# Optimization experiments

Measured on AMD Instinct MI355X. Metric: run time of the kernel, lower is better.

## Reference

```python
import itertools
import jax, jax.numpy as jnp
import numpy as np

# ---- config (mirrors init_kwargs) ----
BS = 8; H = 120; W = 160
RES = 5; ZRES = 5
MAP_SIZE_CM = 2400 // 2          # global_downscaling = 2 -> 1200 cm
VR = 100                          # vision_range
FOV = 79.0
NSEM = 16
CAT_THR = 5.0; EXP_THR = 1.0; MAP_THR = 1.0
AGENT_H = 0.88 * 100.0            # camera height in cm
MAX_H = int(360 / ZRES)           # 72
MIN_H = int(-40 / ZRES)           # -8
MAP_DIM = MAP_SIZE_CM // RES      # 240
XC = (W - 1.0) / 2.0
ZC = (H - 1.0) / 2.0
FL = (W / 2.0) / np.tan(np.deg2rad(FOV / 2.0))
D2R = 1.0 / 57.29577951308232


def splat_feat_nd(init_grid, feat, coords):
    """Trilinear splat-scatter. init_grid: (B,F,*gd); feat: (B,F,P); coords: (B,ndim,P) in [-1,1]."""
    B, Fc = init_grid.shape[:2]
    gd = init_grid.shape[2:]
    n = len(gd)
    grid_flat = init_grid.reshape(B, Fc, -1)
    pos_d, wts_d = [], []
    for d in range(n):
        pos = coords[:, d:d + 1, :] * (gd[d] / 2.0) + gd[d] / 2.0  # (B,1,P)
        pd, wd = [], []
        for ix in (0, 1):
            pos_ix = jnp.floor(pos) + ix
            safe = ((pos_ix > 0) & (pos_ix < gd[d])).astype(pos.dtype)
            wd.append((1.0 - jnp.abs(pos - pos_ix)) * safe)
            pd.append((pos_ix * safe).astype(jnp.int32))
        pos_d.append(pd); wts_d.append(wd)
    bidx = jnp.arange(B)[:, None, None]
    fidx = jnp.arange(Fc)[None, :, None]
    for comb in itertools.product((0, 1), repeat=n):
        idx = jnp.zeros_like(pos_d[0][0])
        w = jnp.ones_like(wts_d[0][0])
        for d in range(n):
            idx = idx * gd[d] + pos_d[d][comb[d]]
            w = w * wts_d[d][comb[d]]
        grid_flat = grid_flat.at[bidx, fidx, idx].add(feat * w)
    return jnp.round(grid_flat).reshape(init_grid.shape)


def affine_grid(theta, Ho, Wo):
    """torch F.affine_grid with align_corners=True. theta: (B,2,3) -> (B,Ho,Wo,2)."""
    xs = jnp.linspace(-1.0, 1.0, Wo)
    ys = jnp.linspace(-1.0, 1.0, Ho)
    Xg, Yg = jnp.meshgrid(xs, ys)
    base = jnp.stack([Xg, Yg, jnp.ones_like(Xg)], -1)  # (Ho,Wo,3)
    return jnp.einsum('hwk,bjk->bhwj', base, theta)


def grid_sample(img, grid):
    """Bilinear grid_sample, align_corners=True, zero padding. img: (B,C,Hi,Wi); grid: (B,Ho,Wo,2)."""
    B, C, Hi, Wi = img.shape
    x = (grid[..., 0] + 1.0) * (Wi - 1) / 2.0
    y = (grid[..., 1] + 1.0) * (Hi - 1) / 2.0
    x0 = jnp.floor(x); y0 = jnp.floor(y)
    bidx = jnp.arange(B)[:, None, None, None]
    cidx = jnp.arange(C)[None, :, None, None]

    def tap(ix, iy, w):
        valid = ((ix >= 0) & (ix < Wi) & (iy >= 0) & (iy < Hi)).astype(img.dtype)
        ixc = jnp.clip(ix, 0, Wi - 1).astype(jnp.int32)
        iyc = jnp.clip(iy, 0, Hi - 1).astype(jnp.int32)
        v = img[bidx, cidx, iyc[:, None], ixc[:, None]]  # (B,C,Ho,Wo)
        return v * (w * valid)[:, None]

    out = tap(x0, y0, (x0 + 1 - x) * (y0 + 1 - y))
    out = out + tap(x0 + 1, y0, (x - x0) * (y0 + 1 - y))
    out = out + tap(x0, y0 + 1, (x0 + 1 - x) * (y - y0))
    out = out + tap(x0 + 1, y0 + 1, (x - x0) * (y - y0))
    return out


def _forward(obs, pose_obs, maps_last, poses_last):
    B, c = obs.shape[0], obs.shape[1]
    depth = obs[:, 3]  # (B,H,W), cm

    # point cloud from depth (du.get_point_cloud_from_z_t, du_scale=1)
    gx = jnp.broadcast_to(jnp.arange(W, dtype=depth.dtype)[None, :], (H, W))
    gz = jnp.broadcast_to(jnp.arange(H - 1, -1, -1, dtype=depth.dtype)[:, None], (H, W))
    X = (gx - XC) * depth / FL
    Z = (gz - ZC) * depth / FL
    pc = jnp.stack([X, depth, Z], axis=-1)  # (B,H,W,3)

    # camera elevation rotation about x-axis (view_angles default to 0)
    elev = jnp.zeros((B,), depth.dtype)
    ce, se = jnp.cos(elev), jnp.sin(elev)
    z0 = jnp.zeros_like(ce); o1 = jnp.ones_like(ce)
    Rx = jnp.stack([o1, z0, z0, z0, ce, -se, z0, se, ce], -1).reshape(B, 3, 3)
    pc = jnp.einsum('bhwk,bjk->bhwj', pc, Rx)
    pc = pc.at[..., 2].add(AGENT_H)

    # shift pose: rotate about z by (pi/2 - pi/2) = 0, translate x by vr*res//2
    ang = np.pi / 2.0 - np.pi / 2.0
    Rz = jnp.array([[np.cos(ang), -np.sin(ang), 0.0],
                    [np.sin(ang), np.cos(ang), 0.0],
                    [0.0, 0.0, 1.0]], depth.dtype)
    pc = jnp.einsum('bhwk,jk->bhwj', pc, Rz)
    pc = pc.at[..., 0].add(VR * RES // 2)

    # normalize to [-1,1] voxel coords
    xs = (pc[..., 0] / RES - VR // 2.0) / VR * 2.0
    ys = (pc[..., 1] / RES - VR // 2.0) / VR * 2.0
    zs = (pc[..., 2] / ZRES - (MAX_H + MIN_H) // 2.0) / (MAX_H - MIN_H) * 2.0
    coords = jnp.stack([xs, ys, zs], 1).reshape(B, 3, H * W)

    # feat: channel 0 = ones (occupancy), rest = semantic masks (AvgPool2d(1) = identity)
    feat = jnp.concatenate([jnp.ones((B, 1, H * W), obs.dtype),
                            obs[:, 4:].reshape(B, NSEM, H * W)], axis=1)

    init_grid = jnp.zeros((B, 1 + NSEM, VR, VR, MAX_H - MIN_H), obs.dtype)
    voxels = splat_feat_nd(init_grid, feat, coords).swapaxes(2, 3)

    min_z = int(5 / ZRES - MIN_H)                  # 9
    max_z = int((AGENT_H + 1 + 50) / ZRES - MIN_H)  # 35
    agent_height_proj = voxels[..., min_z:max_z].sum(4)
    all_height_proj = voxels.sum(4)

    fp_map_pred = jnp.clip(agent_height_proj[:, 0:1] / MAP_THR, 0.0, 1.0)
    fp_exp_pred = jnp.clip(all_height_proj[:, 0:1] / EXP_THR, 0.0, 1.0)

    agent_view = jnp.zeros((B, c, MAP_DIM, MAP_DIM), obs.dtype)
    x1 = MAP_SIZE_CM // (RES * 2) - VR // 2; x2 = x1 + VR
    y1 = MAP_SIZE_CM // (RES * 2); y2 = y1 + VR
    agent_view = agent_view.at[:, 0:1, y1:y2, x1:x2].set(fp_map_pred)
    agent_view = agent_view.at[:, 1:2, y1:y2, x1:x2].set(fp_exp_pred)
    agent_view = agent_view.at[:, 4:, y1:y2, x1:x2].set(
        jnp.clip(agent_height_proj[:, 1:] / CAT_THR, 0.0, 1.0))
    # cat_pred_threshold > 5.0 branch is False (threshold == 5.0)

    # pose update (note: torch mutates poses_last in place -> pose_pred aliases current_poses)
    th = poses_last[:, 2] * D2R
    ny = poses_last[:, 1] + pose_obs[:, 0] * jnp.sin(th) + pose_obs[:, 1] * jnp.cos(th)
    nx = poses_last[:, 0] + pose_obs[:, 0] * jnp.cos(th) - pose_obs[:, 1] * jnp.sin(th)
    nt = poses_last[:, 2] + pose_obs[:, 2] * 57.29577951308232
    nt = jnp.fmod(nt - 180.0, 360.0) + 180.0
    nt = jnp.fmod(nt + 180.0, 360.0) - 180.0
    current_poses = jnp.stack([nx, ny, nt], 1)

    st = jax.lax.stop_gradient(current_poses)  # .clone().detach()
    half = MAP_SIZE_CM // (RES * 2)
    st_xy = -(st[:, :2] * 100.0 / RES - half) / half
    st_t = 90.0 - st[:, 2]
    cos_t = jnp.cos(st_t * np.pi / 180.0); sin_t = jnp.sin(st_t * np.pi / 180.0)
    z0 = jnp.zeros_like(cos_t); o1 = jnp.ones_like(cos_t)
    theta1 = jnp.stack([jnp.stack([cos_t, -sin_t, z0], 1),
                        jnp.stack([sin_t, cos_t, z0], 1)], 1)
    theta2 = jnp.stack([jnp.stack([o1, z0, st_xy[:, 0]], 1),
                        jnp.stack([z0, o1, st_xy[:, 1]], 1)], 1)
    rot_grid = affine_grid(theta1, MAP_DIM, MAP_DIM)
    trans_grid = affine_grid(theta2, MAP_DIM, MAP_DIM)
    rotated = grid_sample(agent_view, rot_grid)
    translated = grid_sample(rotated, trans_grid)

    map_pred = jnp.maximum(maps_last, translated)
    return (fp_map_pred, map_pred, current_poses, current_poses)


def setup_inputs() -> dict:
    key = jax.random.key(0)
    k1, k2, k3, k4, k5, k6 = jax.random.split(key, 6)
    obs = jax.random.uniform(k1, (BS, 4 + NSEM, H, W), jnp.float32)
    depth = 50.0 + 300.0 * jax.random.uniform(k2, (BS, H, W), jnp.float32)  # cm
    obs = obs.at[:, 3].set(depth)
    pose_obs = 0.1 * jax.random.normal(k3, (BS, 3), jnp.float32)
    maps_last = jax.random.uniform(k4, (BS, 4 + NSEM, MAP_DIM, MAP_DIM), jnp.float32)
    xy = 4.0 + 4.0 * jax.random.uniform(k5, (BS, 2), jnp.float32)  # meters, inside 12m map
    th = 360.0 * jax.random.uniform(k6, (BS, 1), jnp.float32) - 180.0
    poses_last = jnp.concatenate([xy, th], 1)
    return {"obs": obs, "pose_obs": pose_obs, "maps_last": maps_last, "poses_last": poses_last}


def reference(obs, pose_obs, maps_last, poses_last):
    return _forward(obs, pose_obs, maps_last, poses_last)
```

## Files before the change

kernel.cpp:

```cpp
#include <hip/hip_runtime.h>
#include <math.h>

#define NB 8
#define NH 120
#define NW 160
#define HW (NH*NW)
#define NSEM 16
#define NCH 20
#define VR 100
#define NZ 80
#define NZP 40
#define ZLO 9
#define ZHI 35
#define NZS (ZHI-ZLO)
#define MD 240
#define PC 20
#define YW 64
#define YOFF 8
#define QS0    256.0f
#define QS0INV 0.00390625f
#define QS2    8.0f
#define QS2INV 0.125f
#define PXB 120
#define ACCS 124
#define GPTS 242

__device__ __forceinline__ float clamp01(float v){ return fminf(fmaxf(v, 0.0f), 1.0f); }

struct SplatCoord {
    float wx0, wx1, wy0, wy1, wz0, wz1;
    int   xi0, xi1, yi0, yi1, zi0, zi1;
};
__device__ __forceinline__ void compute_coord(float d, int h, int w, float fl, SplatCoord& sc) {
    float X = ((float)w - 79.5f) * d / fl;
    float Z = ((float)(119 - h) - 59.5f) * d / fl;
    float pcx = X + 250.0f;
    float pcy = d;
    float pcz = Z + 88.0f;
    float posx = ((pcx/5.0f - 50.0f)/100.0f*2.0f)*50.0f + 50.0f;
    float posy = ((pcy/5.0f - 50.0f)/100.0f*2.0f)*50.0f + 50.0f;
    float posz = ((pcz/5.0f - 32.0f)/80.0f*2.0f)*40.0f + 40.0f;
    float f;
    f = floorf(posx);
    { float pi = f;        bool s = (pi > 0.0f) && (pi < 100.0f);
      sc.wx0 = s ? (1.0f - fabsf(posx - pi)) : 0.0f; sc.xi0 = s ? (int)pi : 0; }
    { float pi = f + 1.0f; bool s = (pi > 0.0f) && (pi < 100.0f);
      sc.wx1 = s ? (1.0f - fabsf(posx - pi)) : 0.0f; sc.xi1 = s ? (int)pi : 0; }
    f = floorf(posy);
    { float pi = f;        bool s = (pi > 0.0f) && (pi < 100.0f);
      sc.wy0 = s ? (1.0f - fabsf(posy - pi)) : 0.0f; sc.yi0 = s ? (int)pi : 0; }
    { float pi = f + 1.0f; bool s = (pi > 0.0f) && (pi < 100.0f);
      sc.wy1 = s ? (1.0f - fabsf(posy - pi)) : 0.0f; sc.yi1 = s ? (int)pi : 0; }
    f = floorf(posz);
    { float pi = f;        bool s = (pi > 0.0f) && (pi < 80.0f);
      sc.wz0 = s ? (1.0f - fabsf(posz - pi)) : 0.0f; sc.zi0 = s ? (int)pi : 0; }
    { float pi = f + 1.0f; bool s = (pi > 0.0f) && (pi < 80.0f);
      sc.wz1 = s ? (1.0f - fabsf(posz - pi)) : 0.0f; sc.zi1 = s ? (int)pi : 0; }
}

__global__ void zero_k(uint4* __restrict__ vox0q4, uint4* __restrict__ voxS4) {
    int b = blockIdx.x & 7;
    int i = ((blockIdx.x >> 3) << 8) + threadIdx.x;
    const uint4 z = make_uint4(0u, 0u, 0u, 0u);
    if (i < 64000) {
        vox0q4[(size_t)b*64000 + i] = z;
    } else {
        voxS4[(size_t)b*166400 + (i - 64000)] = z;
    }
}

__global__ void pose_k(const float* __restrict__ pose_obs,
                       const float* __restrict__ poses_last,
                       float* __restrict__ out2, float* __restrict__ out3,
                       float* __restrict__ aux) {
    int b = threadIdx.x;
    if (b >= NB) return;
    const float D2R = 0.017453292519943295f;
    float th = poses_last[b*3+2] * D2R;
    float s = sinf(th), c = cosf(th);
    float ny = poses_last[b*3+1] + pose_obs[b*3+0]*s + pose_obs[b*3+1]*c;
    float nx = poses_last[b*3+0] + pose_obs[b*3+0]*c - pose_obs[b*3+1]*s;
    float nt = poses_last[b*3+2] + pose_obs[b*3+2]*57.29577951308232f;
    nt = fmodf(nt - 180.0f, 360.0f) + 180.0f;
    nt = fmodf(nt + 180.0f, 360.0f) - 180.0f;
    out2[b*3+0] = nx; out2[b*3+1] = ny; out2[b*3+2] = nt;
    out3[b*3+0] = nx; out3[b*3+1] = ny; out3[b*3+2] = nt;
    float stt = 90.0f - nt;
    float rad = stt * D2R;
    float tx = -(nx*100.0f/5.0f - 120.0f)/120.0f;
    float ty = -(ny*100.0f/5.0f - 120.0f)/120.0f;
    float dx = tx * 119.5f;
    float dy = ty * 119.5f;
    float Kf = floorf(dx), Lf = floorf(dy);
    aux[b*12+0] = cosf(rad);
    aux[b*12+1] = sinf(rad);
    aux[b*12+2] = Kf;
    aux[b*12+3] = Lf;
    aux[b*12+4] = dx - Kf;
    aux[b*12+5] = dy - Lf;
}

__global__ void splat_k(const float* __restrict__ obs, unsigned* __restrict__ vox0q,
                        unsigned* __restrict__ voxS, float fl) {
    int b = blockIdx.x & 7;
    int idx = ((blockIdx.x >> 3) << 8) + threadIdx.x;
    if (idx >= HW*4) return;
    int k = idx & 3; int p = idx >> 2;
    int h = p / NW, w = p % NW;
    const float* ob = obs + (size_t)b*NCH*HW;
    float d = ob[3*HW + p];
    SplatCoord sc;
    compute_coord(d, h, w, fl, sc);

    {
        float wxy = ((k & 1) ? sc.wx1 : sc.wx0) * ((k >> 1) ? sc.wy1 : sc.wy0);
        int   xiv = (k & 1) ? sc.xi1 : sc.xi0;
        unsigned ywi = (unsigned)(((k >> 1) ? sc.yi1 : sc.yi0) - YOFF);
        if (wxy != 0.0f && ywi < YW) {
            unsigned q0 = __float2uint_rn(wxy*sc.wz0*QS0);
            unsigned q1 = __float2uint_rn(wxy*sc.wz1*QS0);
            if (q0 | q1) {
                int z0 = sc.zi0, z1 = sc.zi1;
                size_t rowcol = (size_t)ywi*VR + xiv;
                if (q0 && q1 && !(z0 & 1)) {
                    atomicAdd(&vox0q[((size_t)(b*NZP + (z0 >> 1))*YW*VR) + rowcol], q0 | (q1 << 16));
                } else {
                    if (q0) atomicAdd(&vox0q[((size_t)(b*NZP + (z0 >> 1))*YW*VR) + rowcol],
                                      (z0 & 1) ? (q0 << 16) : q0);
                    if (q1) atomicAdd(&vox0q[((size_t)(b*NZP + (z1 >> 1))*YW*VR) + rowcol],
                                      (z1 & 1) ? (q1 << 16) : q1);
                }
            }
        }
    }

    float f0 = ob[(4 + 4*k + 0)*HW + p];
    float f1 = ob[(4 + 4*k + 1)*HW + p];
    float f2 = ob[(4 + 4*k + 2)*HW + p];
    float f3 = ob[(4 + 4*k + 3)*HW + p];
    #pragma unroll
    for (int cz = 0; cz < 2; cz++) {
        int z = cz ? sc.zi1 : sc.zi0;
        float wzv = cz ? sc.wz1 : sc.wz0;
        if (z < ZLO || z >= ZHI) continue;
        #pragma unroll
        for (int cy = 0; cy < 2; cy++) {
            float wyz = (cy ? sc.wy1 : sc.wy0) * wzv;
            unsigned ywi = (unsigned)((cy ? sc.yi1 : sc.yi0) - YOFF);
            if (ywi >= YW) continue;
            #pragma unroll
            for (int cx = 0; cx < 2; cx++) {
                float w3 = (cx ? sc.wx1 : sc.wx0) * wyz;
                int xiv = cx ? sc.xi1 : sc.xi0;
                if (w3 == 0.0f) continue;
                unsigned q0 = __float2uint_rn(f0*w3*QS2);
                unsigned q1 = __float2uint_rn(f1*w3*QS2);
                unsigned q2 = __float2uint_rn(f2*w3*QS2);
                unsigned q3 = __float2uint_rn(f3*w3*QS2);
                unsigned val = q0 | (q1 << 8) | (q2 << 16) | (q3 << 24);
                if (val) {
                    size_t addr = (((((size_t)b*NZS + (z-ZLO))*YW + ywi)*VR + xiv)<<2) + k;
                    atomicAdd(&voxS[addr], val);
                }
            }
        }
    }
}

__global__ void proj_k(const unsigned* __restrict__ vox0q, const unsigned* __restrict__ voxS,
                       float* __restrict__ proj, float* __restrict__ out0) {
    int b = blockIdx.x & 7;
    int t2 = ((blockIdx.x >> 3) << 8) + threadIdx.x;
    if (t2 < VR*VR) {
        int r = t2;
        int yy = r / VR;
        float* pb = proj + ((size_t)b*(VR*VR) + r)*PC;
        if (yy < YOFF || yy >= YOFF+YW) {
            out0[(size_t)b*(VR*VR) + r] = 0.0f;
            *reinterpret_cast<float2*>(pb) = make_float2(0.0f, 0.0f);
            return;
        }
        int rw = (yy - YOFF)*VR + (r % VR);
        const unsigned* col = vox0q + (size_t)b*NZP*(YW*VR) + rw;
        float s_all = 0.0f, s_slab = 0.0f;
        #pragma unroll
        for (int zp = 0; zp < NZP; zp++) {
            unsigned v = col[(size_t)zp*(YW*VR)];
            float v0 = rintf((float)(v & 0xFFFFu)*QS0INV);
            float v1 = rintf((float)(v >> 16)*QS0INV);
            s_all += v0 + v1;
            if (zp >= 5 && zp <= 16) s_slab += v0 + v1;
            else if (zp == 4) s_slab += v1;
            else if (zp == 17) s_slab += v0;
        }
        float fpm = clamp01(s_slab);
        float fpe = clamp01(s_all);
        out0[(size_t)b*(VR*VR) + r] = fpm;
        *reinterpret_cast<float2*>(pb) = make_float2(fpm, fpe);
        return;
    }
    int r = t2 - VR*VR;
    if (r >= VR*VR) return;
    int yy = r / VR;
    float* dst = proj + ((size_t)b*(VR*VR) + r)*PC + 4;
    if (yy < YOFF || yy >= YOFF+YW) {
        *reinterpret_cast<float4*>(dst)      = make_float4(0.0f, 0.0f, 0.0f, 0.0f);
        *reinterpret_cast<float4*>(dst + 4)  = make_float4(0.0f, 0.0f, 0.0f, 0.0f);
        *reinterpret_cast<float4*>(dst + 8)  = make_float4(0.0f, 0.0f, 0.0f, 0.0f);
        *reinterpret_cast<float4*>(dst + 12) = make_float4(0.0f, 0.0f, 0.0f, 0.0f);
        return;
    }
    int rw = (yy - YOFF)*VR + (r % VR);
    float a00=0.f,a01=0.f,a02=0.f,a03=0.f, a10=0.f,a11=0.f,a12=0.f,a13=0.f;
    float a20=0.f,a21=0.f,a22=0.f,a23=0.f, a30=0.f,a31=0.f,a32=0.f,a33=0.f;
    #pragma unroll 13
    for (int zs = 0; zs < NZS; zs++) {
        const uint4 v = *reinterpret_cast<const uint4*>(
            voxS + ((((size_t)b*NZS + zs)*(YW*VR) + rw)<<2));
        a00 += rintf((float)( v.x        & 0xFFu)*QS2INV);
        a01 += rintf((float)((v.x >>  8) & 0xFFu)*QS2INV);
        a02 += rintf((float)((v.x >> 16) & 0xFFu)*QS2INV);
        a03 += rintf((float)( v.x >> 24         )*QS2INV);
        a10 += rintf((float)( v.y        & 0xFFu)*QS2INV);
        a11 += rintf((float)((v.y >>  8) & 0xFFu)*QS2INV);
        a12 += rintf((float)((v.y >> 16) & 0xFFu)*QS2INV);
        a13 += rintf((float)( v.y >> 24         )*QS2INV);
        a20 += rintf((float)( v.z        & 0xFFu)*QS2INV);
        a21 += rintf((float)((v.z >>  8) & 0xFFu)*QS2INV);
        a22 += rintf((float)((v.z >> 16) & 0xFFu)*QS2INV);
        a23 += rintf((float)( v.z >> 24         )*QS2INV);
        a30 += rintf((float)( v.w        & 0xFFu)*QS2INV);
        a31 += rintf((float)((v.w >>  8) & 0xFFu)*QS2INV);
        a32 += rintf((float)((v.w >> 16) & 0xFFu)*QS2INV);
        a33 += rintf((float)( v.w >> 24         )*QS2INV);
    }
    *reinterpret_cast<float4*>(dst) = make_float4(
        clamp01(a00/5.0f), clamp01(a01/5.0f), clamp01(a02/5.0f), clamp01(a03/5.0f));
    *reinterpret_cast<float4*>(dst + 4) = make_float4(
        clamp01(a10/5.0f), clamp01(a11/5.0f), clamp01(a12/5.0f), clamp01(a13/5.0f));
    *reinterpret_cast<float4*>(dst + 8) = make_float4(
        clamp01(a20/5.0f), clamp01(a21/5.0f), clamp01(a22/5.0f), clamp01(a23/5.0f));
    *reinterpret_cast<float4*>(dst + 12) = make_float4(
        clamp01(a30/5.0f), clamp01(a31/5.0f), clamp01(a32/5.0f), clamp01(a33/5.0f));
}

__global__ __launch_bounds__(256) void rottrans_k(const float* __restrict__ proj,
                           const float* __restrict__ aux,
                           const float* __restrict__ maps, float* __restrict__ out1) {
    __shared__ float s_rot[GPTS*20];
    __shared__ unsigned long long s_mix64[1240];
    unsigned long long* s_rtap = s_mix64;
    unsigned* s_glive = (unsigned*)(s_mix64 + GPTS*4);
    float* s_acc = (float*)s_mix64;

    int blk = blockIdx.x;
    int b = blk & 7;
    int rem = blk >> 3;
    int Y = rem % MD;
    int chunk = rem / MD;
    int X0 = chunk * PXB;
    int t = threadIdx.x;

    float ct = aux[b*12+0], st = aux[b*12+1];
    int K = (int)aux[b*12+2], L = (int)aux[b*12+3];
    float fx = aux[b*12+4], fy = aux[b*12+5];

    size_t bbase = (size_t)b*NCH*(MD*MD) + (size_t)Y*MD + X0;
    int it0 = t, it1 = t + 256, it2 = t + 512;
    size_t o0 = bbase + (size_t)(it0/30)*(MD*MD) + (it0%30)*4;
    size_t o1 = bbase + (size_t)(it1/30)*(MD*MD) + (it1%30)*4;
    float4 m0 = *reinterpret_cast<const float4*>(maps + o0);
    float4 m1 = *reinterpret_cast<const float4*>(maps + o1);
    float4 m2 = make_float4(0.f,0.f,0.f,0.f);
    size_t o2 = 0;
    if (it2 < PXB/4*NCH) {
        o2 = bbase + (size_t)(it2/30)*(MD*MD) + (it2%30)*4;
        m2 = *reinterpret_cast<const float4*>(maps + o2);
    }

    if (t < GPTS) {
        int j = (t >= 121) ? 1 : 0;
        int u = t - j*121;
        int U = X0 + K + u;
        int V = Y + L + j;
        unsigned live = 0;
        const float step = 2.0f/239.0f;
        float x2 = 0.0f, y2 = 0.0f;
        bool inr = (U >= 0) && (U < MD) && (V >= 0) && (V < MD);
        if (inr) {
            float Xg2 = (U == MD-1) ? 1.0f : (-1.0f + (float)U*step);
            float Yg2 = (V == MD-1) ? 1.0f : (-1.0f + (float)V*step);
            float ur = ct*Xg2 - st*Yg2;
            float vr = st*Xg2 + ct*Yg2;
            x2 = (ur + 1.0f)*119.5f;
            y2 = (vr + 1.0f)*119.5f;
        }
        float x20 = floorf(x2), y20 = floorf(y2);
        #pragma unroll
        for (int ii = 0; ii < 4; ii++) {
            float jx = x20 + (float)(ii & 1);
            float jy = y20 + (float)(ii >> 1);
            float w2 = ((ii & 1) ? (x2 - x20) : (x20 + 1.0f - x2)) *
                       ((ii >> 1) ? (y2 - y20) : (y20 + 1.0f - y2));
            bool ivalid = inr && (jy >= 120.0f) && (jy < 220.0f) && (jx >= 70.0f) && (jx < 170.0f);
            float w = ivalid ? w2 : 0.0f;
            int  off = ivalid ? (((int)jy - 120)*VR + ((int)jx - 70)) : 0;
            s_rtap[t*4 + ii] = (unsigned long long)(unsigned)off |
                               ((unsigned long long)__float_as_uint(w) << 32);
            live |= (w != 0.0f) ? 1u : 0u;
        }
        s_glive[t] = live;
    }
    __syncthreads();

    const float* pj = proj + (size_t)b*(VR*VR)*PC;
    for (int item = t; item < GPTS*10; item += 256) {
        int g = item / 10, c = item % 10;
        float a0 = 0.0f, a1 = 0.0f;
        if (s_glive[g]) {
            #pragma unroll
            for (int s = 0; s < 4; s++) {
                unsigned long long tap = s_rtap[g*4 + s];
                float w = __uint_as_float((unsigned)(tap >> 32));
                const float2 v2 = *reinterpret_cast<const float2*>(
                    pj + (size_t)(unsigned)tap*PC + c*2);
                a0 += w*v2.x; a1 += w*v2.y;
            }
        }
        s_rot[g*20 + 2*c]     = a0;
        s_rot[g*20 + 2*c + 1] = a1;
    }
    __syncthreads();

    float w00 = (1.0f-fx)*(1.0f-fy), w10 = fx*(1.0f-fy);
    float w01 = (1.0f-fx)*fy,        w11 = fx*fy;
    for (int item = t; item < PXB*5; item += 256) {
        int px = item / 5, q = item % 5;
        const float4 r00 = *reinterpret_cast<const float4*>(s_rot + (px      )*20 + q*4);
        const float4 r10 = *reinterpret_cast<const float4*>(s_rot + (px + 1  )*20 + q*4);
        const float4 r01 = *reinterpret_cast<const float4*>(s_rot + (121 + px    )*20 + q*4);
        const float4 r11 = *reinterpret_cast<const float4*>(s_rot + (121 + px + 1)*20 + q*4);
        float a0 = w00*r00.x + w10*r10.x + w01*r01.x + w11*r11.x;
        float a1 = w00*r00.y + w10*r10.y + w01*r01.y + w11*r11.y;
        float a2 = w00*r00.z + w10*r10.z + w01*r01.z + w11*r11.z;
        float a3 = w00*r00.w + w10*r10.w + w01*r01.w + w11*r11.w;
        s_acc[(4*q+0)*ACCS + px] = a0;
        s_acc[(4*q+1)*ACCS + px] = a1;
        s_acc[(4*q+2)*ACCS + px] = a2;
        s_acc[(4*q+3)*ACCS + px] = a3;
    }
    __syncthreads();

    {
        int ch = it0/30, pq = it0%30;
        float4 r;
        if (ch == 2 || ch == 3) {
            r = make_float4(fmaxf(m0.x,0.f), fmaxf(m0.y,0.f), fmaxf(m0.z,0.f), fmaxf(m0.w,0.f));
        } else {
            const float4 a = *reinterpret_cast<const float4*>(s_acc + ch*ACCS + pq*4);
            r = make_float4(fmaxf(m0.x,a.x), fmaxf(m0.y,a.y), fmaxf(m0.z,a.z), fmaxf(m0.w,a.w));
        }
        *reinterpret_cast<float4*>(out1 + o0) = r;
    }
    {
        int ch = it1/30, pq = it1%30;
        float4 r;
        if (ch == 2 || ch == 3) {
            r = make_float4(fmaxf(m1.x,0.f), fmaxf(m1.y,0.f), fmaxf(m1.z,0.f), fmaxf(m1.w,0.f));
        } else {
            const float4 a = *reinterpret_cast<const float4*>(s_acc + ch*ACCS + pq*4);
            r = make_float4(fmaxf(m1.x,a.x), fmaxf(m1.y,a.y), fmaxf(m1.z,a.z), fmaxf(m1.w,a.w));
        }
        *reinterpret_cast<float4*>(out1 + o1) = r;
    }
    if (it2 < PXB/4*NCH) {
        int ch = it2/30, pq = it2%30;
        float4 r;
        if (ch == 2 || ch == 3) {
            r = make_float4(fmaxf(m2.x,0.f), fmaxf(m2.y,0.f), fmaxf(m2.z,0.f), fmaxf(m2.w,0.f));
        } else {
            const float4 a = *reinterpret_cast<const float4*>(s_acc + ch*ACCS + pq*4);
            r = make_float4(fmaxf(m2.x,a.x), fmaxf(m2.y,a.y), fmaxf(m2.z,a.z), fmaxf(m2.w,a.w));
        }
        *reinterpret_cast<float4*>(out1 + o2) = r;
    }
}

extern "C" void kernel_launch(void* const* d_in, const int* in_sizes, int n_in,
                              void* d_out, int out_size, void* d_ws, size_t ws_size,
                              hipStream_t stream) {
    const float* obs        = (const float*)d_in[0];
    const float* pose_obs   = (const float*)d_in[1];
    const float* maps_last  = (const float*)d_in[2];
    const float* poses_last = (const float*)d_in[3];
    float* out  = (float*)d_out;
    float* out0 = out;
    float* out1 = out + 80000;
    float* out2 = out + 80000 + 9216000;
    float* out3 = out2 + 24;

    unsigned* vox0q = (unsigned*)d_ws;
    unsigned* voxS  = (unsigned*)d_ws + 2048000;
    float*    proj  = (float*)d_ws + 2048000 + 5324800;
    float*    aux   = proj + 1600000;

    const float FLf = (float)(80.0 / tan(39.5 * M_PI / 180.0));

    zero_k    <<<900*8, 256, 0, stream>>>((uint4*)vox0q, (uint4*)voxS);
    pose_k    <<<1, 64, 0, stream>>>(pose_obs, poses_last, out2, out3, aux);
    splat_k   <<<300*8, 256, 0, stream>>>(obs, vox0q, voxS, FLf);
    proj_k    <<<79*8, 256, 0, stream>>>(vox0q, voxS, proj, out0);
    rottrans_k<<<480*8, 256, 0, stream>>>(proj, aux, maps_last, out1);
}
```

Before: 82.00 us.

## Widen splat atomics to 64-bit and vectorize rotation gather to float4

The splat kernel now gives each thread half of the semantic channels (eight packed 8-bit values) and issues 64-bit atomic adds instead of 32-bit ones. This halves the thread count and the number of atomics, and each thread handles both x-corners for the count voxels. The rotation gather in rottrans now reads float4 instead of float2 per tap, halving its load instructions. The risks are lower parallelism in splat, more registers per thread, and whether 64-bit atomic adds are fast on this hardware.

New measurement: 92.10 us. 1.12x slower.

```diff
diff --git a/kernel.cpp b/kernel.cpp
--- a/kernel.cpp
+++ b/kernel.cpp
@@ -101,43 +101,51 @@
 }
 
 __global__ void splat_k(const float* __restrict__ obs, unsigned* __restrict__ vox0q,
-                        unsigned* __restrict__ voxS, float fl) {
+                        unsigned long long* __restrict__ voxS64, float fl) {
     int b = blockIdx.x & 7;
     int idx = ((blockIdx.x >> 3) << 8) + threadIdx.x;
-    if (idx >= HW*4) return;
-    int k = idx & 3; int p = idx >> 2;
+    if (idx >= HW*2) return;
+    int hf = idx & 1; int p = idx >> 1;
     int h = p / NW, w = p % NW;
     const float* ob = obs + (size_t)b*NCH*HW;
     float d = ob[3*HW + p];
     SplatCoord sc;
     compute_coord(d, h, w, fl, sc);
 
-    {
-        float wxy = ((k & 1) ? sc.wx1 : sc.wx0) * ((k >> 1) ? sc.wy1 : sc.wy0);
-        int   xiv = (k & 1) ? sc.xi1 : sc.xi0;
-        unsigned ywi = (unsigned)(((k >> 1) ? sc.yi1 : sc.yi0) - YOFF);
-        if (wxy != 0.0f && ywi < YW) {
+    float wyv = hf ? sc.wy1 : sc.wy0;
+    unsigned ywi = (unsigned)((hf ? sc.yi1 : sc.yi0) - YOFF);
+    bool yok = (wyv != 0.0f) && (ywi < YW);
+
+    if (yok) {
+        #pragma unroll
+        for (int cx = 0; cx < 2; cx++) {
+            float wxy = (cx ? sc.wx1 : sc.wx0) * wyv;
+            int   xiv = cx ? sc.xi1 : sc.xi0;
+            if (wxy == 0.0f) continue;
             unsigned q0 = __float2uint_rn(wxy*sc.wz0*QS0);
             unsigned q1 = __float2uint_rn(wxy*sc.wz1*QS0);
-            if (q0 | q1) {
-                int z0 = sc.zi0, z1 = sc.zi1;
-                size_t rowcol = (size_t)ywi*VR + xiv;
-                if (q0 && q1 && !(z0 & 1)) {
-                    atomicAdd(&vox0q[((size_t)(b*NZP + (z0 >> 1))*YW*VR) + rowcol], q0 | (q1 << 16));
-                } else {
-                    if (q0) atomicAdd(&vox0q[((size_t)(b*NZP + (z0 >> 1))*YW*VR) + rowcol],
-                                      (z0 & 1) ? (q0 << 16) : q0);
-                    if (q1) atomicAdd(&vox0q[((size_t)(b*NZP + (z1 >> 1))*YW*VR) + rowcol],
-                                      (z1 & 1) ? (q1 << 16) : q1);
-                }
+            if (!(q0 | q1)) continue;
+            int z0 = sc.zi0, z1 = sc.zi1;
+            size_t rowcol = (size_t)ywi*VR + xiv;
+            if (q0 && q1 && !(z0 & 1)) {
+                atomicAdd(&vox0q[((size_t)(b*NZP + (z0 >> 1))*YW*VR) + rowcol], q0 | (q1 << 16));
+            } else {
+                if (q0) atomicAdd(&vox0q[((size_t)(b*NZP + (z0 >> 1))*YW*VR) + rowcol],
+                                  (z0 & 1) ? (q0 << 16) : q0);
+                if (q1) atomicAdd(&vox0q[((size_t)(b*NZP + (z1 >> 1))*YW*VR) + rowcol],
+                                  (z1 & 1) ? (q1 << 16) : q1);
             }
         }
     }
 
-    float f0 = ob[(4 + 4*k + 0)*HW + p];
-    float f1 = ob[(4 + 4*k + 1)*HW + p];
-    float f2 = ob[(4 + 4*k + 2)*HW + p];
-    float f3 = ob[(4 + 4*k + 3)*HW + p];
+    float f0 = ob[(4 + 8*hf + 0)*HW + p];
+    float f1 = ob[(4 + 8*hf + 1)*HW + p];
+    float f2 = ob[(4 + 8*hf + 2)*HW + p];
+    float f3 = ob[(4 + 8*hf + 3)*HW + p];
+    float f4 = ob[(4 + 8*hf + 4)*HW + p];
+    float f5 = ob[(4 + 8*hf + 5)*HW + p];
+    float f6 = ob[(4 + 8*hf + 6)*HW + p];
+    float f7 = ob[(4 + 8*hf + 7)*HW + p];
     #pragma unroll
     for (int cz = 0; cz < 2; cz++) {
         int z = cz ? sc.zi1 : sc.zi0;
@@ -146,21 +154,25 @@
         #pragma unroll
         for (int cy = 0; cy < 2; cy++) {
             float wyz = (cy ? sc.wy1 : sc.wy0) * wzv;
-            unsigned ywi = (unsigned)((cy ? sc.yi1 : sc.yi0) - YOFF);
-            if (ywi >= YW) continue;
+            unsigned ywi2 = (unsigned)((cy ? sc.yi1 : sc.yi0) - YOFF);
+            if (ywi2 >= YW) continue;
             #pragma unroll
             for (int cx = 0; cx < 2; cx++) {
                 float w3 = (cx ? sc.wx1 : sc.wx0) * wyz;
                 int xiv = cx ? sc.xi1 : sc.xi0;
                 if (w3 == 0.0f) continue;
-                unsigned q0 = __float2uint_rn(f0*w3*QS2);
-                unsigned q1 = __float2uint_rn(f1*w3*QS2);
-                unsigned q2 = __float2uint_rn(f2*w3*QS2);
-                unsigned q3 = __float2uint_rn(f3*w3*QS2);
-                unsigned val = q0 | (q1 << 8) | (q2 << 16) | (q3 << 24);
+                float ws = w3*QS2;
+                unsigned q0 = __float2uint_rn(f0*ws), q1 = __float2uint_rn(f1*ws);
+                unsigned q2 = __float2uint_rn(f2*ws), q3 = __float2uint_rn(f3*ws);
+                unsigned q4 = __float2uint_rn(f4*ws), q5 = __float2uint_rn(f5*ws);
+                unsigned q6 = __float2uint_rn(f6*ws), q7 = __float2uint_rn(f7*ws);
+                unsigned lo = q0 | (q1 << 8) | (q2 << 16) | (q3 << 24);
+                unsigned hi = q4 | (q5 << 8) | (q6 << 16) | (q7 << 24);
+                unsigned long long val = (unsigned long long)lo |
+                                         ((unsigned long long)hi << 32);
                 if (val) {
-                    size_t addr = (((((size_t)b*NZS + (z-ZLO))*YW + ywi)*VR + xiv)<<2) + k;
-                    atomicAdd(&voxS[addr], val);
+                    size_t addr = (((((size_t)b*NZS + (z-ZLO))*YW + ywi2)*VR + xiv)<<1) + hf;
+                    atomicAdd(&voxS64[addr], val);
                 }
             }
         }
@@ -314,21 +326,20 @@
     __syncthreads();
 
     const float* pj = proj + (size_t)b*(VR*VR)*PC;
-    for (int item = t; item < GPTS*10; item += 256) {
-        int g = item / 10, c = item % 10;
-        float a0 = 0.0f, a1 = 0.0f;
+    for (int item = t; item < GPTS*5; item += 256) {
+        int g = item / 5, q = item % 5;
+        float a0 = 0.0f, a1 = 0.0f, a2 = 0.0f, a3 = 0.0f;
         if (s_glive[g]) {
             #pragma unroll
             for (int s = 0; s < 4; s++) {
                 unsigned long long tap = s_rtap[g*4 + s];
                 float w = __uint_as_float((unsigned)(tap >> 32));
-                const float2 v2 = *reinterpret_cast<const float2*>(
-                    pj + (size_t)(unsigned)tap*PC + c*2);
-                a0 += w*v2.x; a1 += w*v2.y;
+                const float4 v4 = *reinterpret_cast<const float4*>(
+                    pj + (size_t)(unsigned)tap*PC + q*4);
+                a0 += w*v4.x; a1 += w*v4.y; a2 += w*v4.z; a3 += w*v4.w;
             }
         }
-        s_rot[g*20 + 2*c]     = a0;
-        s_rot[g*20 + 2*c + 1] = a1;
+        *reinterpret_cast<float4*>(s_rot + g*20 + q*4) = make_float4(a0, a1, a2, a3);
     }
     __syncthreads();
 
@@ -408,7 +419,7 @@
 
     zero_k    <<<900*8, 256, 0, stream>>>((uint4*)vox0q, (uint4*)voxS);
     pose_k    <<<1, 64, 0, stream>>>(pose_obs, poses_last, out2, out3, aux);
-    splat_k   <<<300*8, 256, 0, stream>>>(obs, vox0q, voxS, FLf);
+    splat_k   <<<150*8, 256, 0, stream>>>(obs, vox0q, (unsigned long long*)voxS, FLf);
     proj_k    <<<79*8, 256, 0, stream>>>(vox0q, voxS, proj, out0);
     rottrans_k<<<480*8, 256, 0, stream>>>(proj, aux, maps_last, out1);
 }
```
